# Optimization experiments

Measured on AMD Instinct MI355X. Metric: run time of the kernel, lower is better.

The kernel has to match this reference:

```python
import jax, jax.numpy as jnp
import numpy as np

N_NODES = 50000
N_EDGES = 1600000
N_FEATS = 8
D_HID = 64


def setup_inputs() -> dict:
    key = jax.random.key(0)
    ks = jax.random.split(key, 8)
    X = jax.random.normal(ks[0], (N_NODES, N_FEATS), dtype=jnp.float32)
    edge_index = jax.random.randint(ks[1], (2, N_EDGES), 0, N_NODES, dtype=jnp.int64)
    # two filter taps per layer, torch.rand init -> uniform [0,1)
    H0_0 = jax.random.uniform(ks[2], (1, D_HID), dtype=jnp.float32)
    H0_1 = jax.random.uniform(ks[3], (1, D_HID), dtype=jnp.float32)
    H1_0 = jax.random.uniform(ks[4], (D_HID, D_HID), dtype=jnp.float32)
    H1_1 = jax.random.uniform(ks[5], (D_HID, D_HID), dtype=jnp.float32)
    H2_0 = jax.random.uniform(ks[6], (D_HID, 1), dtype=jnp.float32)
    H2_1 = jax.random.uniform(ks[7], (D_HID, 1), dtype=jnp.float32)
    return {"X": X, "edge_index": edge_index,
            "H0_0": H0_0, "H0_1": H0_1,
            "H1_0": H1_0, "H1_1": H1_1,
            "H2_0": H2_0, "H2_1": H2_1}


def reference(X, edge_index, H0_0, H0_1, H1_0, H1_1, H2_0, H2_1):
    n = X.shape[0]
    row, col = edge_index[0], edge_index[1]
    # GCN-style symmetric normalization based on target-node degree (PyG degree(col, N))
    deg = jax.ops.segment_sum(jnp.ones_like(col, dtype=X.dtype), col, num_segments=n)
    dinv = jnp.where(deg > 0, jax.lax.rsqrt(deg), 0.0)
    norm = (dinv[row] * dinv[col])[:, None]  # [E,1]

    def conv(x, Ha, Hb):
        # x: [N, in_dim]; out = x@Ha + scatter_add(norm * (x@Hb)[row] -> col)
        x1 = x @ Ha
        x2 = x @ Hb
        agg = jax.ops.segment_sum(norm * x2[row], col, num_segments=n)
        return x1 + agg

    def per_col(xc):  # xc: [N, 1] -> [N]
        h = jax.nn.elu(conv(xc, H0_0, H0_1))
        h = jax.nn.elu(conv(h, H1_0, H1_1))
        out = conv(h, H2_0, H2_1)
        return out[:, 0]

    # Columns are independent (original Python loop over X.shape[1]);
    # lax.map bounds peak memory to one column's E x D_HID message tensor.
    cols = jax.lax.map(per_col, jnp.moveaxis(X, 1, 0)[..., None])  # [F, N]
    return cols.T  # [N, F]
```

## Files before the change

kernel.cpp:

```cpp
#include <hip/hip_runtime.h>
#include <hip/hip_bf16.h>
#include <math.h>

typedef __hip_bfloat16 bf16;
typedef unsigned int uint;
typedef unsigned short ushort;
typedef __attribute__((ext_vector_type(8))) short short8;
typedef __attribute__((ext_vector_type(4))) float f32x4;

__device__ inline float blo(uint u) { return __uint_as_float(u << 16); }
__device__ inline float bhi(uint u) { return __uint_as_float(u & 0xffff0000u); }
__device__ inline short f2bf(float v) {
    bf16 t = __float2bfloat16(v);
    short r;
    __builtin_memcpy(&r, &t, 2);
    return r;
}
__device__ inline uint bpack(float a, float b) {
    return (uint)(ushort)f2bf(a) | ((uint)(ushort)f2bf(b) << 16);
}
__device__ inline float eluf(float v) { return v > 0.0f ? v : (__expf(v) - 1.0f); }


__global__ void k_zero_i32(int* p, int n) {
    int i = blockIdx.x * blockDim.x + threadIdx.x;
    if (i < n) p[i] = 0;
}

__global__ void k_telemetry(float* out, int n, float v) {
    int i = blockIdx.x * blockDim.x + threadIdx.x;
    if (i < n) out[i] = v;
}

__global__ void k_wt(const float* __restrict__ W, ushort* __restrict__ Wt) {
    int i = blockIdx.x * blockDim.x + threadIdx.x;
    if (i >= 4096) return;
    int k = i >> 6, c = i & 63;
    Wt[c * 64 + k] = (ushort)f2bf(W[i]);
}


__global__ void __launch_bounds__(256) k_count2(const int* __restrict__ col,
                                                int* __restrict__ deg, int E, int N) {
    int slot = blockIdx.x & 7;
    int per = (N + 7) >> 3;
    int lo = slot * per;
    int hi = min(N, lo + per);
    int stride = (gridDim.x >> 3) * 256;
    for (int e = (blockIdx.x >> 3) * 256 + threadIdx.x; e < E; e += stride) {
        int c = col[e];
        if (c >= lo && c < hi) atomicAdd(&deg[c], 1);
    }
}

__global__ void k_dinv(const int* __restrict__ deg, float* __restrict__ dinv, int N) {
    int n = blockIdx.x * blockDim.x + threadIdx.x;
    if (n < N) {
        int d = deg[n];
        dinv[n] = d > 0 ? rsqrtf((float)d) : 0.0f;
    }
}

__global__ void k_scan_block(const int* in, int* incl, int* bsums, int N) {
    __shared__ int sh[256];
    int i = blockIdx.x * 256 + threadIdx.x;
    int v = (i < N) ? in[i] : 0;
    sh[threadIdx.x] = v;
    __syncthreads();
    for (int ofs = 1; ofs < 256; ofs <<= 1) {
        int t = (threadIdx.x >= ofs) ? sh[threadIdx.x - ofs] : 0;
        __syncthreads();
        sh[threadIdx.x] += t;
        __syncthreads();
    }
    if (i < N) incl[i] = sh[threadIdx.x];
    if (threadIdx.x == 255) bsums[blockIdx.x] = sh[255];
}

__global__ void k_scan_sums(int* bsums, int nb) {
    __shared__ int sh[256];
    int v = (threadIdx.x < (unsigned)nb) ? bsums[threadIdx.x] : 0;
    sh[threadIdx.x] = v;
    __syncthreads();
    for (int ofs = 1; ofs < 256; ofs <<= 1) {
        int t = (threadIdx.x >= ofs) ? sh[threadIdx.x - ofs] : 0;
        __syncthreads();
        sh[threadIdx.x] += t;
        __syncthreads();
    }
    if (threadIdx.x < (unsigned)nb) bsums[threadIdx.x] = sh[threadIdx.x] - v;
}

__global__ void k_finalize(const int* incl, const int* deg, const int* bexcl,
                           int* off, int* cursor, int N, int E) {
    int i = blockIdx.x * blockDim.x + threadIdx.x;
    if (i < N) {
        int ex = incl[i] - deg[i] + bexcl[i >> 8];
        off[i] = ex;
        cursor[i] = ex;
    }
    if (i == 0) off[N] = E;
}

__global__ void __launch_bounds__(256) k_fill2(const int* __restrict__ ei, int* cursor,
                                               int* __restrict__ srow, int E, int N) {
    int slot = blockIdx.x & 7;
    int per = (N + 7) >> 3;
    int lo = slot * per;
    int hi = min(N, lo + per);
    int stride = (gridDim.x >> 3) * 256;
    for (int e = (blockIdx.x >> 3) * 256 + threadIdx.x; e < E; e += stride) {
        int c = ei[E + e];
        if (c < lo || c >= hi) continue;
        int r = ei[e];
        int pos = atomicAdd(&cursor[c], 1);
        srow[pos] = r;
    }
}


__global__ void __launch_bounds__(256) k_sgat2(const int* __restrict__ off,
                                               const int* __restrict__ srow,
                                               const float* __restrict__ dinv,
                                               const float* __restrict__ X,
                                               float* __restrict__ s, int N) {
    int wid = (blockIdx.x * 256 + threadIdx.x) >> 6;
    int lane = threadIdx.x & 63;
    if (wid >= N) return;
    int a = off[wid], b = off[wid + 1];
    int grp = lane >> 1, sub = lane & 1;
    float4 acc = make_float4(0.f, 0.f, 0.f, 0.f);
    for (int i = a + grp; i < b; i += 32) {
        int r = srow[i];
        float dr = dinv[r];
        float4 v = *(const float4*)(X + (size_t)r * 8 + sub * 4);
        acc.x += dr * v.x; acc.y += dr * v.y; acc.z += dr * v.z; acc.w += dr * v.w;
    }
#pragma unroll
    for (int ofs = 2; ofs < 64; ofs <<= 1) {
        acc.x += __shfl_xor(acc.x, ofs);
        acc.y += __shfl_xor(acc.y, ofs);
        acc.z += __shfl_xor(acc.z, ofs);
        acc.w += __shfl_xor(acc.w, ofs);
    }
    if (lane < 2) {
        float dc = dinv[wid];
        float4 o = make_float4(dc * acc.x, dc * acc.y, dc * acc.z, dc * acc.w);
        *(float4*)(s + (size_t)wid * 8 + sub * 4) = o;
    }
}


__global__ void __launch_bounds__(256) k_mfma8(const float* __restrict__ Xf,
                                               const float* __restrict__ sf,
                                               const float* __restrict__ W0a,
                                               const float* __restrict__ W0b,
                                               const ushort* __restrict__ W10t,
                                               const ushort* __restrict__ W11t,
                                               const float* __restrict__ dinv,
                                               char* __restrict__ m8,
                                               float* __restrict__ smax,
                                               ushort* __restrict__ p, int R) {
    int w = threadIdx.x >> 6;
    int l = threadIdx.x & 63;
    int r16 = l & 15;
    int kg = l >> 4;
    int row = blockIdx.x * 64 + w * 16 + r16;
    float x = 0.f, sv = 0.f;
    if (row < R) { x = Xf[row]; sv = sf[row]; }

    short8 afr[2];
#pragma unroll
    for (int kk = 0; kk < 2; ++kk) {
        int k0 = kk * 32 + kg * 8;
        float4 wa0 = *(const float4*)(W0a + k0);
        float4 wa1 = *(const float4*)(W0a + k0 + 4);
        float4 wb0 = *(const float4*)(W0b + k0);
        float4 wb1 = *(const float4*)(W0b + k0 + 4);
        afr[kk][0] = f2bf(eluf(x * wa0.x + sv * wb0.x));
        afr[kk][1] = f2bf(eluf(x * wa0.y + sv * wb0.y));
        afr[kk][2] = f2bf(eluf(x * wa0.z + sv * wb0.z));
        afr[kk][3] = f2bf(eluf(x * wa0.w + sv * wb0.w));
        afr[kk][4] = f2bf(eluf(x * wa1.x + sv * wb1.x));
        afr[kk][5] = f2bf(eluf(x * wa1.y + sv * wb1.y));
        afr[kk][6] = f2bf(eluf(x * wa1.z + sv * wb1.z));
        afr[kk][7] = f2bf(eluf(x * wa1.w + sv * wb1.w));
    }

    f32x4 accM[4], accP[4];
#pragma unroll
    for (int ct = 0; ct < 4; ++ct) {
        accM[ct] = (f32x4)(0.f);
        accP[ct] = (f32x4)(0.f);
    }
#pragma unroll
    for (int kk = 0; kk < 2; ++kk) {
        int k0 = kk * 32 + kg * 8;
#pragma unroll
        for (int ct = 0; ct < 4; ++ct) {
            int bcol = ct * 16 + r16;
            short8 bm = *(const short8*)(W11t + bcol * 64 + k0);
            short8 bp = *(const short8*)(W10t + bcol * 64 + k0);
            accM[ct] = __builtin_amdgcn_mfma_f32_16x16x32_bf16(afr[kk], bm, accM[ct], 0, 0, 0);
            accP[ct] = __builtin_amdgcn_mfma_f32_16x16x32_bf16(afr[kk], bp, accP[ct], 0, 0, 0);
        }
    }
#pragma unroll
    for (int reg = 0; reg < 4; ++reg) {
        int grow = blockIdx.x * 64 + w * 16 + kg * 4 + reg;
        if (grow >= R) continue;
        float dv = dinv[grow >> 3];
        float mx = fmaxf(fmaxf(fabsf(accM[0][reg]), fabsf(accM[1][reg])),
                         fmaxf(fabsf(accM[2][reg]), fabsf(accM[3][reg])));
#pragma unroll
        for (int ofs = 1; ofs < 16; ofs <<= 1) mx = fmaxf(mx, __shfl_xor(mx, ofs));
        float qinv = mx > 0.f ? 127.0f / mx : 0.f;
#pragma unroll
        for (int ct = 0; ct < 4; ++ct) {
            int col = ct * 16 + r16;
            int q = __float2int_rn(accM[ct][reg] * qinv);
            m8[(size_t)grow * 64 + col] = (char)q;
            p[(size_t)grow * 64 + col] = (ushort)f2bf(accP[ct][reg]);
        }
        if (r16 == 0) smax[grow] = dv * mx * (1.0f / 127.0f);
    }
}


__global__ void __launch_bounds__(256) k_gth_all8(const int* __restrict__ off,
                                                  const int* __restrict__ srow,
                                                  const float* __restrict__ dinv,
                                                  const char* __restrict__ m8,
                                                  const float* __restrict__ smax,
                                                  const uint* __restrict__ p_all,
                                                  const float* __restrict__ W2a,
                                                  const float* __restrict__ W2b,
                                                  float* __restrict__ T, float* __restrict__ U,
                                                  int N) {
    int wid = (blockIdx.x * 256 + threadIdx.x) >> 6;
    int lane = threadIdx.x & 63;
    if (wid >= N) return;
    int a = off[wid], b = off[wid + 1];
    int cc = lane >> 3, d0 = (lane & 7) * 8;
    float acc[8];
#pragma unroll
    for (int j = 0; j < 8; ++j) acc[j] = 0.f;

#define ACC8(vv, sc)                                                        \
    {                                                                       \
        uint lo = (vv).x, hi = (vv).y;                                      \
        acc[0] += (sc) * (float)((int)(lo << 24) >> 24);                    \
        acc[1] += (sc) * (float)((int)(lo << 16) >> 24);                    \
        acc[2] += (sc) * (float)((int)(lo << 8) >> 24);                     \
        acc[3] += (sc) * (float)((int)lo >> 24);                            \
        acc[4] += (sc) * (float)((int)(hi << 24) >> 24);                    \
        acc[5] += (sc) * (float)((int)(hi << 16) >> 24);                    \
        acc[6] += (sc) * (float)((int)(hi << 8) >> 24);                     \
        acc[7] += (sc) * (float)((int)hi >> 24);                            \
    }

    int i = a;
    for (; i + 3 < b; i += 4) {
        int r0 = srow[i], r1 = srow[i + 1], r2 = srow[i + 2], r3 = srow[i + 3];
        uint2 v0 = *(const uint2*)(m8 + (size_t)r0 * 512 + lane * 8);
        uint2 v1 = *(const uint2*)(m8 + (size_t)r1 * 512 + lane * 8);
        uint2 v2 = *(const uint2*)(m8 + (size_t)r2 * 512 + lane * 8);
        uint2 v3 = *(const uint2*)(m8 + (size_t)r3 * 512 + lane * 8);
        float s0 = smax[r0 * 8 + cc];
        float s1 = smax[r1 * 8 + cc];
        float s2 = smax[r2 * 8 + cc];
        float s3 = smax[r3 * 8 + cc];
        ACC8(v0, s0)
        ACC8(v1, s1)
        ACC8(v2, s2)
        ACC8(v3, s3)
    }
    for (; i < b; ++i) {
        int r0 = srow[i];
        uint2 v0 = *(const uint2*)(m8 + (size_t)r0 * 512 + lane * 8);
        float s0 = smax[r0 * 8 + cc];
        ACC8(v0, s0)
    }
#undef ACC8

    float dv = dinv[wid];
    uint4 pv = *(const uint4*)(p_all + ((size_t)wid * 8 + cc) * 32 + (lane & 7) * 4);
    float pa[8] = {blo(pv.x), bhi(pv.x), blo(pv.y), bhi(pv.y),
                   blo(pv.z), bhi(pv.z), blo(pv.w), bhi(pv.w)};
    float tp = 0.f, up = 0.f;
#pragma unroll
    for (int j = 0; j < 8; ++j) {
        float h2 = eluf(pa[j] + dv * acc[j]);
        tp += h2 * W2a[d0 + j];
        up += h2 * W2b[d0 + j];
    }
#pragma unroll
    for (int ofs = 1; ofs < 8; ofs <<= 1) {
        tp += __shfl_xor(tp, ofs);
        up += __shfl_xor(up, ofs);
    }
    if ((lane & 7) == 0) {
        T[(size_t)wid * 8 + cc] = tp;
        U[(size_t)wid * 8 + cc] = dv * up;
    }
}


__global__ void __launch_bounds__(256) k_pre(const float* __restrict__ X,
                                             const float* __restrict__ s,
                                             const float* __restrict__ W0a,
                                             const float* __restrict__ W0b,
                                             const float* __restrict__ W10,
                                             const float* __restrict__ W11,
                                             const float* __restrict__ dinv,
                                             uint* __restrict__ m, uint* __restrict__ p,
                                             int N, int c) {
    __shared__ float w0[64][64];
    __shared__ float w1[64][64];
    __shared__ float hsm[64][65];
    int n0 = blockIdx.x * 64;
    for (int i = threadIdx.x; i < 4096; i += 256) {
        w0[i >> 6][i & 63] = W10[i];
        w1[i >> 6][i & 63] = W11[i];
    }
    int pair = threadIdx.x >> 3;
    int db = (threadIdx.x & 7) * 8;
    __syncthreads();
    for (int i = threadIdx.x; i < 512; i += 256) {
        int nl = i >> 3, qd = i & 7;
        int n = n0 + nl;
        float x = 0.f, sv = 0.f;
        if (n < N) { x = X[(size_t)n * 8 + c]; sv = s[(size_t)n * 8 + c]; }
#pragma unroll
        for (int j = 0; j < 8; ++j) {
            float v = x * W0a[qd * 8 + j] + sv * W0b[qd * 8 + j];
            hsm[nl][qd * 8 + j] = eluf(v);
        }
    }
    __syncthreads();
    float am[2][8], ap[2][8];
#pragma unroll
    for (int j = 0; j < 8; ++j) { am[0][j] = am[1][j] = ap[0][j] = ap[1][j] = 0.f; }
    for (int k = 0; k < 64; ++k) {
        float h0v = hsm[pair * 2][k];
        float h1v = hsm[pair * 2 + 1][k];
#pragma unroll
        for (int j = 0; j < 8; ++j) {
            float wm = w1[k][db + j], wp = w0[k][db + j];
            am[0][j] += h0v * wm; am[1][j] += h1v * wm;
            ap[0][j] += h0v * wp; ap[1][j] += h1v * wp;
        }
    }
#pragma unroll
    for (int tt = 0; tt < 2; ++tt) {
        int n = n0 + pair * 2 + tt;
        if (n < N) {
            float dv = dinv[n];
            size_t ro = (size_t)n * 32 + (db >> 1);
            uint4 om;
            om.x = bpack(dv * am[tt][0], dv * am[tt][1]);
            om.y = bpack(dv * am[tt][2], dv * am[tt][3]);
            om.z = bpack(dv * am[tt][4], dv * am[tt][5]);
            om.w = bpack(dv * am[tt][6], dv * am[tt][7]);
            *(uint4*)(m + ro) = om;
            uint4 op;
            op.x = bpack(ap[tt][0], ap[tt][1]);
            op.y = bpack(ap[tt][2], ap[tt][3]);
            op.z = bpack(ap[tt][4], ap[tt][5]);
            op.w = bpack(ap[tt][6], ap[tt][7]);
            *(uint4*)(p + ro) = op;
        }
    }
}


__global__ void __launch_bounds__(256) k_gth_col(const int* __restrict__ off,
                                                 const int* __restrict__ srow,
                                                 const float* __restrict__ dinv,
                                                 const uint* __restrict__ m,
                                                 const uint* __restrict__ p,
                                                 const float* __restrict__ W2a,
                                                 const float* __restrict__ W2b,
                                                 float* __restrict__ T, float* __restrict__ U,
                                                 int N, int c) {
    int wid = (blockIdx.x * 256 + threadIdx.x) >> 6;
    int lane = threadIdx.x & 63;
    if (wid >= N) return;
    int a = off[wid], b = off[wid + 1];
    int grp = lane >> 3, sub = lane & 7;
    float acc[8];
#pragma unroll
    for (int j = 0; j < 8; ++j) acc[j] = 0.f;
    int i = a + grp;
    for (; i + 8 < b; i += 16) {
        int r0 = srow[i], r1 = srow[i + 8];
        uint4 v0 = *(const uint4*)(m + (size_t)r0 * 32 + sub * 4);
        uint4 v1 = *(const uint4*)(m + (size_t)r1 * 32 + sub * 4);
        acc[0] += blo(v0.x); acc[1] += bhi(v0.x);
        acc[2] += blo(v0.y); acc[3] += bhi(v0.y);
        acc[4] += blo(v0.z); acc[5] += bhi(v0.z);
        acc[6] += blo(v0.w); acc[7] += bhi(v0.w);
        acc[0] += blo(v1.x); acc[1] += bhi(v1.x);
        acc[2] += blo(v1.y); acc[3] += bhi(v1.y);
        acc[4] += blo(v1.z); acc[5] += bhi(v1.z);
        acc[6] += blo(v1.w); acc[7] += bhi(v1.w);
    }
    if (i < b) {
        int r0 = srow[i];
        uint4 v0 = *(const uint4*)(m + (size_t)r0 * 32 + sub * 4);
        acc[0] += blo(v0.x); acc[1] += bhi(v0.x);
        acc[2] += blo(v0.y); acc[3] += bhi(v0.y);
        acc[4] += blo(v0.z); acc[5] += bhi(v0.z);
        acc[6] += blo(v0.w); acc[7] += bhi(v0.w);
    }
#pragma unroll
    for (int ofs = 8; ofs < 64; ofs <<= 1) {
#pragma unroll
        for (int j = 0; j < 8; ++j) acc[j] += __shfl_xor(acc[j], ofs);
    }
    float dv = dinv[wid];
    uint4 pv = *(const uint4*)(p + (size_t)wid * 32 + sub * 4);
    float pa[8] = {blo(pv.x), bhi(pv.x), blo(pv.y), bhi(pv.y),
                   blo(pv.z), bhi(pv.z), blo(pv.w), bhi(pv.w)};
    float tp = 0.f, up = 0.f;
#pragma unroll
    for (int j = 0; j < 8; ++j) {
        float h2 = eluf(pa[j] + dv * acc[j]);
        tp += h2 * W2a[sub * 8 + j];
        up += h2 * W2b[sub * 8 + j];
    }
#pragma unroll
    for (int ofs = 1; ofs < 8; ofs <<= 1) {
        tp += __shfl_xor(tp, ofs);
        up += __shfl_xor(up, ofs);
    }
    if (lane == 0) {
        T[(size_t)wid * 8 + c] = tp;
        U[(size_t)wid * 8 + c] = dv * up;
    }
}


__global__ void __launch_bounds__(256) k_outall(const int* __restrict__ off,
                                                const int* __restrict__ srow,
                                                const float* __restrict__ dinv,
                                                const float* __restrict__ T,
                                                const float* __restrict__ U,
                                                float* __restrict__ out, int N) {
    int wid = (blockIdx.x * 256 + threadIdx.x) >> 6;
    int lane = threadIdx.x & 63;
    if (wid >= N) return;
    int a = off[wid], b = off[wid + 1];
    int grp = lane >> 1, sub = lane & 1;
    float4 acc = make_float4(0.f, 0.f, 0.f, 0.f);
    for (int i = a + grp; i < b; i += 32) {
        int r = srow[i];
        float4 v = *(const float4*)(U + (size_t)r * 8 + sub * 4);
        acc.x += v.x; acc.y += v.y; acc.z += v.z; acc.w += v.w;
    }
#pragma unroll
    for (int ofs = 2; ofs < 64; ofs <<= 1) {
        acc.x += __shfl_xor(acc.x, ofs);
        acc.y += __shfl_xor(acc.y, ofs);
        acc.z += __shfl_xor(acc.z, ofs);
        acc.w += __shfl_xor(acc.w, ofs);
    }
    if (lane < 2) {
        float dv = dinv[wid];
        float4 tv = *(const float4*)(T + (size_t)wid * 8 + sub * 4);
        float4 o = make_float4(tv.x + dv * acc.x, tv.y + dv * acc.y,
                               tv.z + dv * acc.z, tv.w + dv * acc.w);
        *(float4*)(out + (size_t)wid * 8 + sub * 4) = o;
    }
}


extern "C" void kernel_launch(void* const* d_in, const int* in_sizes, int n_in,
                              void* d_out, int out_size, void* d_ws, size_t ws_size,
                              hipStream_t stream) {
    const float* X = (const float*)d_in[0];
    const int* ei = (const int*)d_in[1];
    const float* H00 = (const float*)d_in[2];
    const float* H01 = (const float*)d_in[3];
    const float* H10 = (const float*)d_in[4];
    const float* H11 = (const float*)d_in[5];
    const float* H20 = (const float*)d_in[6];
    const float* H21 = (const float*)d_in[7];
    float* out = (float*)d_out;

    const int N = in_sizes[0] / 8;
    const int E = in_sizes[1] / 2;
    const int R = N * 8;

    size_t pos = 0;
    auto A = [&](size_t bytes) -> size_t {
        size_t r = pos;
        pos += (bytes + 255) & ~(size_t)255;
        return r;
    };
    size_t o_off   = A((size_t)(N + 1) * 4);
    size_t o_dinv  = A((size_t)N * 4);
    size_t o_deg   = A((size_t)N * 4);
    size_t o_incl  = A((size_t)N * 4);
    size_t o_bsums = A(1024);
    size_t o_srow  = A((size_t)E * 4);
    size_t o_s     = A((size_t)N * 8 * 4);
    size_t o_T     = A((size_t)N * 8 * 4);
    size_t o_U     = A((size_t)N * 8 * 4);
    size_t o_w10t  = A(4096 * 2);
    size_t o_w11t  = A(4096 * 2);
    size_t fixed_end = pos;

    size_t need_big = fixed_end + (((size_t)R * 128 + 255) & ~(size_t)255)
                                + (((size_t)R * 64 + 255) & ~(size_t)255)
                                + (((size_t)R * 4 + 255) & ~(size_t)255);
    bool BIG = (ws_size >= need_big);

    size_t o_p, o_m8, o_smax, o_m;
    if (BIG) {
        o_p    = A((size_t)R * 128);
        o_m8   = A((size_t)R * 64);
        o_smax = A((size_t)R * 4);
        o_m    = 0;
    } else {
        o_m = A((size_t)N * 64 * 2);
        o_p = A((size_t)N * 64 * 2);
        o_m8 = o_smax = 0;
    }
    size_t needed = pos;

    if (ws_size < needed) {
        float v = 1.0e9f + (float)(ws_size >> 20) * 1.0e6f;
        k_telemetry<<<(N * 8 + 255) / 256, 256, 0, stream>>>(out, N * 8, v);
        return;
    }

    char* base = (char*)d_ws;
    int*    off    = (int*)(base + o_off);
    float*  dinv   = (float*)(base + o_dinv);
    int*    deg    = (int*)(base + o_deg);
    int*    incl   = (int*)(base + o_incl);
    int*    cursor = incl;
    int*    bsums  = (int*)(base + o_bsums);
    int*    srow   = (int*)(base + o_srow);
    float*  s      = (float*)(base + o_s);
    float*  T      = (float*)(base + o_T);
    float*  U      = (float*)(base + o_U);
    ushort* W10t   = (ushort*)(base + o_w10t);
    ushort* W11t   = (ushort*)(base + o_w11t);

    int nb = (N + 255) / 256;
    int wb = (N * 64 + 255) / 256;

    k_zero_i32<<<nb, 256, 0, stream>>>(deg, N);
    k_count2<<<8 * 1024, 256, 0, stream>>>(ei + E, deg, E, N);
    k_dinv<<<nb, 256, 0, stream>>>(deg, dinv, N);
    k_scan_block<<<nb, 256, 0, stream>>>(deg, incl, bsums, N);
    k_scan_sums<<<1, 256, 0, stream>>>(bsums, nb);
    k_finalize<<<nb, 256, 0, stream>>>(incl, deg, bsums, off, cursor, N, E);
    k_fill2<<<8 * 1024, 256, 0, stream>>>(ei, cursor, srow, E, N);
    k_sgat2<<<wb, 256, 0, stream>>>(off, srow, dinv, X, s, N);
    k_wt<<<16, 256, 0, stream>>>(H10, W10t);
    k_wt<<<16, 256, 0, stream>>>(H11, W11t);

    if (BIG) {
        ushort* p    = (ushort*)(base + o_p);
        char*   m8   = (char*)(base + o_m8);
        float*  smax = (float*)(base + o_smax);
        k_mfma8<<<(R + 63) / 64, 256, 0, stream>>>(X, s, H00, H01, W10t, W11t, dinv,
                                                   m8, smax, p, R);
        k_gth_all8<<<wb, 256, 0, stream>>>(off, srow, dinv, m8, smax, (const uint*)p,
                                           H20, H21, T, U, N);
    } else {
        ushort* m = (ushort*)(base + o_m);
        ushort* p = (ushort*)(base + o_p);
        for (int c = 0; c < 8; ++c) {
            k_pre<<<(N + 63) / 64, 256, 0, stream>>>(X, s, H00, H01, H10, H11, dinv,
                                                     (uint*)m, (uint*)p, N, c);
            k_gth_col<<<wb, 256, 0, stream>>>(off, srow, dinv, (const uint*)m, (const uint*)p,
                                              H20, H21, T, U, N, c);
        }
    }
    k_outall<<<wb, 256, 0, stream>>>(off, srow, dinv, T, U, out, N);
}
```

Measured before the change: 395.1 us.

## Split gather into two half-column passes with two edge slots per wave

The int8 message gather is split into two launches, each covering four of the eight columns. Within a wave, the two 32-lane halves handle alternating edges and combine their partial sums with a cross-half shuffle. Each pass touches a 256-byte half of every source row, which shrinks the per-pass working set so it fits better in cache, and it doubles the independent edge loads in flight per lane group. The cost is reading srow and off twice and adding a launch. Separately, dinv is now computed inside the scan kernel and the two weight-transpose launches are merged into one.

Measured after the change: 408.4 us. 3.4% more time.

```diff
diff --git a/kernel.cpp b/kernel.cpp
--- a/kernel.cpp
+++ b/kernel.cpp
@@ -32,11 +32,13 @@
     if (i < n) out[i] = v;
 }
 
-__global__ void k_wt(const float* __restrict__ W, ushort* __restrict__ Wt) {
+__global__ void k_wt2(const float* __restrict__ W10, const float* __restrict__ W11,
+                      ushort* __restrict__ W10t, ushort* __restrict__ W11t) {
     int i = blockIdx.x * blockDim.x + threadIdx.x;
     if (i >= 4096) return;
     int k = i >> 6, c = i & 63;
-    Wt[c * 64 + k] = (ushort)f2bf(W[i]);
+    W10t[c * 64 + k] = (ushort)f2bf(W10[i]);
+    W11t[c * 64 + k] = (ushort)f2bf(W11[i]);
 }
 
 
@@ -53,18 +55,12 @@
     }
 }
 
-__global__ void k_dinv(const int* __restrict__ deg, float* __restrict__ dinv, int N) {
-    int n = blockIdx.x * blockDim.x + threadIdx.x;
-    if (n < N) {
-        int d = deg[n];
-        dinv[n] = d > 0 ? rsqrtf((float)d) : 0.0f;
-    }
-}
-
-__global__ void k_scan_block(const int* in, int* incl, int* bsums, int N) {
+__global__ void k_scan_block(const int* in, int* incl, int* bsums,
+                             float* __restrict__ dinv, int N) {
     __shared__ int sh[256];
     int i = blockIdx.x * 256 + threadIdx.x;
     int v = (i < N) ? in[i] : 0;
+    if (i < N) dinv[i] = v > 0 ? rsqrtf((float)v) : 0.0f;
     sh[threadIdx.x] = v;
     __syncthreads();
     for (int ofs = 1; ofs < 256; ofs <<= 1) {
@@ -227,7 +223,7 @@
 }
 
 
-__global__ void __launch_bounds__(256) k_gth_all8(const int* __restrict__ off,
+__global__ void __launch_bounds__(256) k_gth_half(const int* __restrict__ off,
                                                   const int* __restrict__ srow,
                                                   const float* __restrict__ dinv,
                                                   const char* __restrict__ m8,
@@ -236,12 +232,16 @@
                                                   const float* __restrict__ W2a,
                                                   const float* __restrict__ W2b,
                                                   float* __restrict__ T, float* __restrict__ U,
-                                                  int N) {
+                                                  int N, int cbase) {
     int wid = (blockIdx.x * 256 + threadIdx.x) >> 6;
     int lane = threadIdx.x & 63;
     if (wid >= N) return;
     int a = off[wid], b = off[wid + 1];
-    int cc = lane >> 3, d0 = (lane & 7) * 8;
+    int eslot = lane >> 5;
+    int cq = (lane >> 3) & 3;
+    int sub = lane & 7;
+    int col = cbase + cq;
+    size_t boff = (size_t)col * 64 + sub * 8;
     float acc[8];
 #pragma unroll
     for (int j = 0; j < 8; ++j) acc[j] = 0.f;
@@ -259,49 +259,46 @@
         acc[7] += (sc) * (float)((int)hi >> 24);                            \
     }
 
-    int i = a;
-    for (; i + 3 < b; i += 4) {
-        int r0 = srow[i], r1 = srow[i + 1], r2 = srow[i + 2], r3 = srow[i + 3];
-        uint2 v0 = *(const uint2*)(m8 + (size_t)r0 * 512 + lane * 8);
-        uint2 v1 = *(const uint2*)(m8 + (size_t)r1 * 512 + lane * 8);
-        uint2 v2 = *(const uint2*)(m8 + (size_t)r2 * 512 + lane * 8);
-        uint2 v3 = *(const uint2*)(m8 + (size_t)r3 * 512 + lane * 8);
-        float s0 = smax[r0 * 8 + cc];
-        float s1 = smax[r1 * 8 + cc];
-        float s2 = smax[r2 * 8 + cc];
-        float s3 = smax[r3 * 8 + cc];
+    int i = a + eslot;
+    for (; i + 2 < b; i += 4) {
+        int r0 = srow[i], r1 = srow[i + 2];
+        uint2 v0 = *(const uint2*)(m8 + (size_t)r0 * 512 + boff);
+        uint2 v1 = *(const uint2*)(m8 + (size_t)r1 * 512 + boff);
+        float s0 = smax[r0 * 8 + col];
+        float s1 = smax[r1 * 8 + col];
         ACC8(v0, s0)
         ACC8(v1, s1)
-        ACC8(v2, s2)
-        ACC8(v3, s3)
-    }
-    for (; i < b; ++i) {
+    }
+    if (i < b) {
         int r0 = srow[i];
-        uint2 v0 = *(const uint2*)(m8 + (size_t)r0 * 512 + lane * 8);
-        float s0 = smax[r0 * 8 + cc];
+        uint2 v0 = *(const uint2*)(m8 + (size_t)r0 * 512 + boff);
+        float s0 = smax[r0 * 8 + col];
         ACC8(v0, s0)
     }
 #undef ACC8
 
-    float dv = dinv[wid];
-    uint4 pv = *(const uint4*)(p_all + ((size_t)wid * 8 + cc) * 32 + (lane & 7) * 4);
-    float pa[8] = {blo(pv.x), bhi(pv.x), blo(pv.y), bhi(pv.y),
-                   blo(pv.z), bhi(pv.z), blo(pv.w), bhi(pv.w)};
-    float tp = 0.f, up = 0.f;
-#pragma unroll
-    for (int j = 0; j < 8; ++j) {
-        float h2 = eluf(pa[j] + dv * acc[j]);
-        tp += h2 * W2a[d0 + j];
-        up += h2 * W2b[d0 + j];
-    }
-#pragma unroll
-    for (int ofs = 1; ofs < 8; ofs <<= 1) {
-        tp += __shfl_xor(tp, ofs);
-        up += __shfl_xor(up, ofs);
-    }
-    if ((lane & 7) == 0) {
-        T[(size_t)wid * 8 + cc] = tp;
-        U[(size_t)wid * 8 + cc] = dv * up;
+#pragma unroll
+    for (int j = 0; j < 8; ++j) acc[j] += __shfl_xor(acc[j], 32);
+
+    if (lane < 32) {
+        float dv = dinv[wid];
+        uint4 pv = *(const uint4*)(p_all + ((size_t)wid * 8 + col) * 32 + sub * 4);
+        float pa[8] = {blo(pv.x), bhi(pv.x), blo(pv.y), bhi(pv.y),
+                       blo(pv.z), bhi(pv.z), blo(pv.w), bhi(pv.w)};
+        float tp = 0.f, up = 0.f;
+#pragma unroll
+        for (int j = 0; j < 8; ++j) {
+            float h2 = eluf(pa[j] + dv * acc[j]);
+            tp += h2 * W2a[sub * 8 + j];
+            up += h2 * W2b[sub * 8 + j];
+        }
+        tp += __shfl_xor(tp, 1); up += __shfl_xor(up, 1);
+        tp += __shfl_xor(tp, 2); up += __shfl_xor(up, 2);
+        tp += __shfl_xor(tp, 4); up += __shfl_xor(up, 4);
+        if (sub == 0) {
+            T[(size_t)wid * 8 + col] = tp;
+            U[(size_t)wid * 8 + col] = dv * up;
+        }
     }
 }
 
@@ -554,14 +551,12 @@
 
     k_zero_i32<<<nb, 256, 0, stream>>>(deg, N);
     k_count2<<<8 * 1024, 256, 0, stream>>>(ei + E, deg, E, N);
-    k_dinv<<<nb, 256, 0, stream>>>(deg, dinv, N);
-    k_scan_block<<<nb, 256, 0, stream>>>(deg, incl, bsums, N);
+    k_scan_block<<<nb, 256, 0, stream>>>(deg, incl, bsums, dinv, N);
     k_scan_sums<<<1, 256, 0, stream>>>(bsums, nb);
     k_finalize<<<nb, 256, 0, stream>>>(incl, deg, bsums, off, cursor, N, E);
     k_fill2<<<8 * 1024, 256, 0, stream>>>(ei, cursor, srow, E, N);
     k_sgat2<<<wb, 256, 0, stream>>>(off, srow, dinv, X, s, N);
-    k_wt<<<16, 256, 0, stream>>>(H10, W10t);
-    k_wt<<<16, 256, 0, stream>>>(H11, W11t);
+    k_wt2<<<16, 256, 0, stream>>>(H10, H11, W10t, W11t);
 
     if (BIG) {
         ushort* p    = (ushort*)(base + o_p);
@@ -569,8 +564,10 @@
         float*  smax = (float*)(base + o_smax);
         k_mfma8<<<(R + 63) / 64, 256, 0, stream>>>(X, s, H00, H01, W10t, W11t, dinv,
                                                    m8, smax, p, R);
-        k_gth_all8<<<wb, 256, 0, stream>>>(off, srow, dinv, m8, smax, (const uint*)p,
-                                           H20, H21, T, U, N);
+        k_gth_half<<<wb, 256, 0, stream>>>(off, srow, dinv, m8, smax, (const uint*)p,
+                                           H20, H21, T, U, N, 0);
+        k_gth_half<<<wb, 256, 0, stream>>>(off, srow, dinv, m8, smax, (const uint*)p,
+                                           H20, H21, T, U, N, 4);
     } else {
         ushort* m = (ushort*)(base + o_m);
         ushort* p = (ushort*)(base + o_p);
```
